# Optimization experiments

Hardware: AMD Instinct MI355X
Metric: run time of the kernel (lower is better)

The kernel has to match this reference:

```python
import jax, jax.numpy as jnp
import numpy as np

N = 20000   # nodes
E = 200000  # edges
D = 32      # inp_dim == out_dim == emb_dim
R = 100     # num_rel
EPS = 1e-5  # BatchNorm1d default eps


def setup_inputs() -> dict:
    key = jax.random.key(0)
    ks = jax.random.split(key, 5)
    h = jax.random.normal(ks[0], (N, D), dtype=jnp.float32)
    # xavier_uniform-ish scale for [R, D, D] relation weights
    weight = jax.random.normal(ks[1], (R, D, D), dtype=jnp.float32) * (1.0 / np.sqrt(D))
    gamma = jnp.ones((D,), dtype=jnp.float32)
    beta = jnp.zeros((D,), dtype=jnp.float32)
    src = jax.random.randint(ks[2], (E,), 0, N, dtype=jnp.int32)
    dst = jax.random.randint(ks[3], (E,), 0, N, dtype=jnp.int32)
    etype = jax.random.randint(ks[4], (E,), 0, R, dtype=jnp.int32)
    return {"h": h, "weight": weight, "gamma": gamma, "beta": beta,
            "src": src, "dst": dst, "etype": etype}


def reference(h, weight, gamma, beta, src, dst, etype):
    # per-edge relation-weight gather: [E, D, D]
    w_e = weight[etype]
    # per-edge bmm (src feature row-vector @ relation matrix) + relu: [E, D]
    msg = jax.nn.relu(jnp.einsum('ed,edo->eo', h[src], w_e))
    # BatchNorm1d in training mode: batch stats over the edge dimension
    mu = jnp.mean(msg, axis=0)
    var = jnp.mean(jnp.square(msg - mu), axis=0)  # biased variance
    msg = (msg - mu) * jax.lax.rsqrt(var + EPS) * gamma + beta
    # segment-mean reduce of messages into destination nodes: [N, D]
    ssum = jax.ops.segment_sum(msg, dst, num_segments=N)
    cnt = jax.ops.segment_sum(jnp.ones((E,), msg.dtype), dst, num_segments=N)
    return ssum / jnp.maximum(cnt, 1.0)[:, None]
```

## Files before the change

### kernel.cpp

```cpp
#include <hip/hip_runtime.h>

#define D 32
#define EPS 1e-5f
#define TPB 256
#define NB 256
#define NSLOT 64


__global__ void hist3_kernel(const int* __restrict__ etype, const int* __restrict__ dst,
                             int E, int R, int chunk,
                             int* __restrict__ blockHistT,
                             int* __restrict__ cnt)
{
    __shared__ int lh[1024];
    for (int i = threadIdx.x; i < R; i += TPB) lh[i] = 0;
    __syncthreads();
    const int lo = blockIdx.x * chunk, hi = min(E, lo + chunk);
    for (int e = lo + threadIdx.x; e < hi; e += TPB) {
        atomicAdd(&lh[etype[e]], 1);
        atomicAdd(&cnt[dst[e]], 1);
    }
    __syncthreads();
    for (int r = threadIdx.x; r < R; r += TPB)
        blockHistT[r * NB + blockIdx.x] = lh[r];
}

__global__ __launch_bounds__(TPB)
void scanA_kernel(int* __restrict__ blockHistT, int* __restrict__ relTot)
{
    const int r = blockIdx.x;
    const int t = threadIdx.x;
    __shared__ int s[TPB];
    const int v = blockHistT[r * NB + t];
    s[t] = v;
    __syncthreads();
    for (int off = 1; off < TPB; off <<= 1) {
        const int u = (t >= off) ? s[t - off] : 0;
        __syncthreads();
        s[t] += u;
        __syncthreads();
    }
    blockHistT[r * NB + t] = s[t] - v;
    if (t == TPB - 1) relTot[r] = s[t];
}

__global__ __launch_bounds__(1024)
void scanB_kernel(const int* __restrict__ relTot, int R, int E, int N,
                  int* __restrict__ rel_start,
                  int* __restrict__ task_rel, int* __restrict__ task_start,
                  int* __restrict__ n_tasks,
                  const int* __restrict__ cnt,
                  int* __restrict__ dst_base, int* __restrict__ cursor_dst)
{
    const int t = threadIdx.x;
    __shared__ int sa[1024];
    __shared__ int sc[1024];
    __shared__ int sb[1024];

    const int tot = (t < R) ? relTot[t] : 0;
    const int nb  = (tot + TPB - 1) / TPB;
    sa[t] = tot; sc[t] = nb;
    __syncthreads();
    for (int off = 1; off < 1024; off <<= 1) {
        const int va = (t >= off) ? sa[t - off] : 0;
        const int vc = (t >= off) ? sc[t - off] : 0;
        __syncthreads();
        sa[t] += va; sc[t] += vc;
        __syncthreads();
    }
    if (t < R) {
        const int st = sa[t] - tot;
        const int tb = sc[t] - nb;
        rel_start[t] = st;
        for (int b = 0; b < nb; ++b) {
            task_rel[tb + b]   = t;
            task_start[tb + b] = st + b * TPB;
        }
    }
    if (t == R - 1) {
        rel_start[R] = sa[t];
        *n_tasks = sc[t];
    }

    const int chunk = (N + 1023) >> 10;
    const int lo = t * chunk, hi = min(N, lo + chunk);
    int part = 0;
    for (int i = lo; i < hi; ++i) part += cnt[i];
    sb[t] = part;
    __syncthreads();
    for (int off = 1; off < 1024; off <<= 1) {
        const int v = (t >= off) ? sb[t - off] : 0;
        __syncthreads();
        sb[t] += v;
        __syncthreads();
    }
    int base = sb[t] - part;
    for (int i = lo; i < hi; ++i) {
        dst_base[i]   = base;
        cursor_dst[i] = base;
        base += cnt[i];
    }
    if (t == 0) dst_base[N] = E;
}

__global__ void scatter3_kernel(const int* __restrict__ src, const int* __restrict__ dst,
                                const int* __restrict__ etype, int E, int R, int chunk,
                                const int* __restrict__ blockHistT,
                                const int* __restrict__ rel_start,
                                int* __restrict__ cursor_dst,
                                int* __restrict__ ssrc, int* __restrict__ perm)
{
    __shared__ int cur[1024];
    for (int r = threadIdx.x; r < R; r += TPB)
        cur[r] = rel_start[r] + blockHistT[r * NB + blockIdx.x];
    __syncthreads();
    const int lo = blockIdx.x * chunk, hi = min(E, lo + chunk);
    for (int e = lo + threadIdx.x; e < hi; e += TPB) {
        const int p = atomicAdd(&cur[etype[e]], 1);
        ssrc[p] = src[e];
        const int q = atomicAdd(&cursor_dst[dst[e]], 1);
        perm[q] = p;
    }
}

__global__ __launch_bounds__(TPB)
void rgcn_main3(const float* __restrict__ h, const float* __restrict__ W,
                const int* __restrict__ rel_start,
                const int* __restrict__ task_rel, const int* __restrict__ task_start,
                const int* __restrict__ n_tasks_p,
                const int* __restrict__ ssrc,
                float* __restrict__ msg,
                float* __restrict__ stat_part)
{
    __shared__ float s_tile[TPB * 33];
    __shared__ int   s_src[TPB];
    __shared__ float s_aux[2 * TPB];

    const int task = blockIdx.x;
    if (task >= *n_tasks_p) return;
    const int r      = task_rel[task];
    const int start  = task_start[task];
    const int relEnd = rel_start[r + 1];
    const int nE     = min(TPB, relEnd - start);
    const int tid    = threadIdx.x;

    if (tid < nE) s_src[tid] = ssrc[start + tid];
    __syncthreads();

    for (int i = tid; i < nE * 8; i += TPB) {
        const int row = i >> 3, seg = i & 7;
        const float4 v = *(const float4*)(h + (size_t)s_src[row] * D + seg * 4);
        float* p = &s_tile[row * 33 + seg * 4];
        p[0] = v.x; p[1] = v.y; p[2] = v.z; p[3] = v.w;
    }
    __syncthreads();

    const float* Wr = W + (size_t)__builtin_amdgcn_readfirstlane(r) * (D * D);

    float acc[D];
#pragma unroll
    for (int o = 0; o < D; ++o) acc[o] = 0.f;

    if (tid < nE) {
#pragma unroll 4
        for (int d = 0; d < D; ++d) {
            const float hd = s_tile[tid * 33 + d];
#pragma unroll
            for (int o = 0; o < D; ++o)
                acc[o] = fmaf(hd, Wr[d * D + o], acc[o]);
        }
#pragma unroll
        for (int o = 0; o < D; ++o) acc[o] = fmaxf(acc[o], 0.f);
    }
    __syncthreads();

    if (tid < nE) {
#pragma unroll
        for (int o = 0; o < D; ++o) s_tile[tid * 33 + o] = acc[o];
    }
    __syncthreads();

    float* mbase = msg + (size_t)start * D;
    float ps = 0.f, pq = 0.f;
    for (int i = tid; i < nE * D; i += TPB) {
        const int row = i >> 5, o = i & 31;
        const float v = s_tile[row * 33 + o];
        mbase[i] = v;
        ps += v; pq += v * v;
    }
    s_aux[tid]       = ps;
    s_aux[TPB + tid] = pq;
    __syncthreads();
    if (tid < D) {
        float ss = 0.f, sq = 0.f;
#pragma unroll
        for (int c = 0; c < TPB / D; ++c) {
            ss += s_aux[c * D + tid];
            sq += s_aux[TPB + c * D + tid];
        }
        float* sp = stat_part + (size_t)(blockIdx.x & (NSLOT - 1)) * (2 * D);
        atomicAdd(&sp[tid],     ss);
        atomicAdd(&sp[D + tid], sq);
    }
}

__global__ __launch_bounds__(TPB)
void reduce3_kernel(const float* __restrict__ msg, const int* __restrict__ perm,
                    const int* __restrict__ dst_base,
                    const float* __restrict__ stat_part,
                    const float* __restrict__ gamma, const float* __restrict__ beta,
                    float invE, int N, float* __restrict__ out)
{
    __shared__ float s_sc[D], s_sh[D];
    const int tid = threadIdx.x;
    if (tid < D) {
        float ss = 0.f, qq = 0.f;
#pragma unroll 4
        for (int s = 0; s < NSLOT; ++s) {
            ss += stat_part[(size_t)s * (2 * D) + tid];
            qq += stat_part[(size_t)s * (2 * D) + D + tid];
        }
        const float mu  = ss * invE;
        const float var = fmaxf(qq * invE - mu * mu, 0.f);
        const float is  = rsqrtf(var + EPS);
        const float sc  = gamma[tid] * is;
        s_sc[tid] = sc;
        s_sh[tid] = fmaf(-mu, sc, beta[tid]);
    }
    __syncthreads();
    const int o    = tid & (D - 1);
    const int node = blockIdx.x * (TPB / D) + (tid >> 5);
    if (node >= N) return;
    const int b0 = dst_base[node], b1 = dst_base[node + 1];
    float v = 0.f;
    for (int q = b0; q < b1; ++q) {
        const int pe = perm[q];
        v += msg[(size_t)pe * D + o];
    }
    const float c = (float)(b1 - b0);
    out[(size_t)node * D + o] = fmaf(v, s_sc[o], s_sh[o] * c) / fmaxf(c, 1.0f);
}


__global__ void hist2_kernel(const int* __restrict__ etype, int E, int R, int chunk,
                             int* __restrict__ blockHistT)
{
    __shared__ int lh[1024];
    for (int i = threadIdx.x; i < R; i += TPB) lh[i] = 0;
    __syncthreads();
    const int lo = blockIdx.x * chunk, hi = min(E, lo + chunk);
    for (int e = lo + threadIdx.x; e < hi; e += TPB)
        atomicAdd(&lh[etype[e]], 1);
    __syncthreads();
    for (int r = threadIdx.x; r < R; r += TPB)
        blockHistT[r * NB + blockIdx.x] = lh[r];
}

__global__ void scan2_kernel(int* __restrict__ blockHistT, int R,
                             int* __restrict__ rel_start,
                             int* __restrict__ task_rel, int* __restrict__ task_start,
                             int* __restrict__ n_tasks)
{
    __shared__ int tot[1024];
    __shared__ int s_start[1025];
    __shared__ int s_tbase[1024];
    const int r = threadIdx.x;
    if (r < R) {
        int acc = 0;
        int* p = blockHistT + r * NB;
        for (int b = 0; b < NB; ++b) { int v = p[b]; p[b] = acc; acc += v; }
        tot[r] = acc;
    }
    __syncthreads();
    if (threadIdx.x == 0) {
        int acc = 0, tb = 0;
        for (int rr = 0; rr < R; ++rr) {
            s_start[rr] = acc; s_tbase[rr] = tb;
            acc += tot[rr];
            tb  += (tot[rr] + TPB - 1) / TPB;
        }
        s_start[R] = acc;
        rel_start[R] = acc;
        *n_tasks = tb;
    }
    __syncthreads();
    if (r < R) {
        const int st = s_start[r];
        rel_start[r] = st;
        const int nb = (tot[r] + TPB - 1) / TPB;
        const int tb = s_tbase[r];
        for (int b = 0; b < nb; ++b) {
            task_rel[tb + b]   = r;
            task_start[tb + b] = st + b * TPB;
        }
    }
}

__global__ void scatter2_kernel(const int* __restrict__ src, const int* __restrict__ dst,
                                const int* __restrict__ etype, int E, int R, int chunk,
                                const int* __restrict__ blockHistT,
                                const int* __restrict__ rel_start,
                                int* __restrict__ ssrc, int* __restrict__ sdst)
{
    __shared__ int cur[1024];
    for (int r = threadIdx.x; r < R; r += TPB)
        cur[r] = rel_start[r] + blockHistT[r * NB + blockIdx.x];
    __syncthreads();
    const int lo = blockIdx.x * chunk, hi = min(E, lo + chunk);
    for (int e = lo + threadIdx.x; e < hi; e += TPB) {
        const int p = atomicAdd(&cur[etype[e]], 1);
        ssrc[p] = src[e];
        sdst[p] = dst[e];
    }
}

__global__ __launch_bounds__(TPB)
void rgcn_main(const float* __restrict__ h, const float* __restrict__ W,
               const int* __restrict__ rel_start,
               const int* __restrict__ task_rel, const int* __restrict__ task_start,
               const int* __restrict__ n_tasks_p,
               const int* __restrict__ ssrc, const int* __restrict__ sdst,
               float* __restrict__ out,
               float* __restrict__ stat_sum, float* __restrict__ stat_sq,
               float* __restrict__ cnt)
{
    __shared__ float s_tile[TPB * 33];
    __shared__ int   s_src[TPB];
    __shared__ int   s_dst[TPB];
    __shared__ float s_aux[2 * TPB];

    const int task = blockIdx.x;
    if (task >= *n_tasks_p) return;
    const int r      = task_rel[task];
    const int start  = task_start[task];
    const int relEnd = rel_start[r + 1];
    const int nE     = min(TPB, relEnd - start);
    const int tid    = threadIdx.x;

    if (tid < nE) {
        s_src[tid] = ssrc[start + tid];
        s_dst[tid] = sdst[start + tid];
    }
    __syncthreads();

    for (int i = tid; i < nE * 8; i += TPB) {
        const int row = i >> 3, seg = i & 7;
        const float4 v = *(const float4*)(h + (size_t)s_src[row] * D + seg * 4);
        float* p = &s_tile[row * 33 + seg * 4];
        p[0] = v.x; p[1] = v.y; p[2] = v.z; p[3] = v.w;
    }
    __syncthreads();

    const float* Wr = W + (size_t)__builtin_amdgcn_readfirstlane(r) * (D * D);

    float acc[D];
#pragma unroll
    for (int o = 0; o < D; ++o) acc[o] = 0.f;

    if (tid < nE) {
#pragma unroll 4
        for (int d = 0; d < D; ++d) {
            const float hd = s_tile[tid * 33 + d];
#pragma unroll
            for (int o = 0; o < D; ++o)
                acc[o] = fmaf(hd, Wr[d * D + o], acc[o]);
        }
#pragma unroll
        for (int o = 0; o < D; ++o) acc[o] = fmaxf(acc[o], 0.f);
        atomicAdd(&cnt[s_dst[tid]], 1.0f);
    }
    __syncthreads();

    if (tid < nE) {
#pragma unroll
        for (int o = 0; o < D; ++o) s_tile[tid * 33 + o] = acc[o];
    }
    __syncthreads();

    float ps = 0.f, pq = 0.f;
    for (int i = tid; i < nE * D; i += TPB) {
        const int row = i >> 5, o = i & 31;
        const float v = s_tile[row * 33 + o];
        atomicAdd(&out[(size_t)s_dst[row] * D + o], v);
        ps += v; pq += v * v;
    }
    s_aux[tid]       = ps;
    s_aux[TPB + tid] = pq;
    __syncthreads();
    if (tid < D) {
        float ss = 0.f, sq = 0.f;
#pragma unroll
        for (int c = 0; c < TPB / D; ++c) {
            ss += s_aux[c * D + tid];
            sq += s_aux[TPB + c * D + tid];
        }
        atomicAdd(&stat_sum[tid], ss);
        atomicAdd(&stat_sq[tid], sq);
    }
}

__global__ void finalize_kernel(float* __restrict__ out, const float* __restrict__ cnt,
                                const float* __restrict__ stat_sum,
                                const float* __restrict__ stat_sq,
                                const float* __restrict__ gamma,
                                const float* __restrict__ beta,
                                float invE, int total)
{
    const int i = blockIdx.x * TPB + threadIdx.x;
    if (i >= total) return;
    const int o    = i & 31;
    const int node = i >> 5;
    const float mu  = stat_sum[o] * invE;
    const float var = fmaxf(stat_sq[o] * invE - mu * mu, 0.f);
    const float is  = rsqrtf(var + EPS);
    const float sc  = gamma[o] * is;
    const float sh  = fmaf(-mu, sc, beta[o]);
    const float c   = cnt[node];
    out[i] = fmaf(out[i], sc, sh * c) / fmaxf(c, 1.0f);
}

extern "C" void kernel_launch(void* const* d_in, const int* in_sizes, int n_in,
                              void* d_out, int out_size, void* d_ws, size_t ws_size,
                              hipStream_t stream)
{
    const float* h     = (const float*)d_in[0];
    const float* W     = (const float*)d_in[1];
    const float* gamma = (const float*)d_in[2];
    const float* beta  = (const float*)d_in[3];
    const int*   src   = (const int*)d_in[4];
    const int*   dst   = (const int*)d_in[5];
    const int*   etype = (const int*)d_in[6];
    float* out = (float*)d_out;

    const int E = in_sizes[4];
    const int N = in_sizes[0] / D;
    const int R = in_sizes[1] / (D * D);
    const int T = R + (E + TPB - 1) / TPB;
    const int chunk = (E + NB - 1) / NB;

    const size_t o_statp      = 0;
    const size_t o_cnt        = o_statp + (size_t)NSLOT * 2 * D;
    const size_t zwords       = o_cnt + (size_t)N;
    const size_t o_relTot     = zwords;
    const size_t o_rel_start  = o_relTot + R;
    const size_t o_n_tasks    = o_rel_start + R + 1;
    const size_t o_task_rel   = o_n_tasks + 1;
    const size_t o_task_start = o_task_rel + T;
    const size_t o_blockHistT = o_task_start + T;
    const size_t o_dst_base   = o_blockHistT + (size_t)R * NB;
    const size_t o_cursor_dst = o_dst_base + N + 1;
    const size_t o_ssrc       = o_cursor_dst + N;
    const size_t o_perm       = o_ssrc + (size_t)E;
    const size_t o_msg        = (o_perm + (size_t)E + 3) & ~(size_t)3;
    const size_t total_words  = o_msg + (size_t)E * D;

    if (R >= 1 && R <= 1024 && NB == TPB && ws_size >= total_words * 4) {
        float* stat_part  = (float*)d_ws + o_statp;
        int*   cnt        = (int*)d_ws + o_cnt;
        int*   relTot     = (int*)d_ws + o_relTot;
        int*   rel_start  = (int*)d_ws + o_rel_start;
        int*   n_tasks    = (int*)d_ws + o_n_tasks;
        int*   task_rel   = (int*)d_ws + o_task_rel;
        int*   task_start = (int*)d_ws + o_task_start;
        int*   blockHistT = (int*)d_ws + o_blockHistT;
        int*   dst_base   = (int*)d_ws + o_dst_base;
        int*   cursor_dst = (int*)d_ws + o_cursor_dst;
        int*   ssrc       = (int*)d_ws + o_ssrc;
        int*   perm       = (int*)d_ws + o_perm;
        float* msg        = (float*)d_ws + o_msg;

        hipMemsetAsync(d_ws, 0, zwords * 4, stream);

        hist3_kernel<<<NB, TPB, 0, stream>>>(etype, dst, E, R, chunk,
                                             blockHistT, cnt);
        scanA_kernel<<<R, TPB, 0, stream>>>(blockHistT, relTot);
        scanB_kernel<<<1, 1024, 0, stream>>>(relTot, R, E, N,
                                             rel_start, task_rel, task_start,
                                             n_tasks, cnt, dst_base, cursor_dst);
        scatter3_kernel<<<NB, TPB, 0, stream>>>(src, dst, etype, E, R, chunk,
                                                blockHistT, rel_start,
                                                cursor_dst, ssrc, perm);
        rgcn_main3<<<T, TPB, 0, stream>>>(h, W, rel_start, task_rel, task_start,
                                          n_tasks, ssrc, msg, stat_part);
        reduce3_kernel<<<(N + TPB / D - 1) / (TPB / D), TPB, 0, stream>>>(
            msg, perm, dst_base, stat_part, gamma, beta,
            1.0f / (float)E, N, out);
        return;
    }

    float* stat_sum  = (float*)d_ws;
    float* stat_sq   = stat_sum + D;
    float* cntf      = stat_sq + D;
    int*   rel_start = (int*)(cntf + N);
    int*   n_tasks   = rel_start + R + 1;
    int*   task_rel  = n_tasks + 1;
    int*   task_start= task_rel + T;
    int*   blockHistT= task_start + T;
    int*   ssrc      = blockHistT + R * NB;
    int*   sdst      = ssrc + E;

    hipMemsetAsync(d_ws, 0, sizeof(float) * (size_t)(2 * D + N), stream);
    hipMemsetAsync(d_out, 0, sizeof(float) * (size_t)out_size, stream);

    hist2_kernel<<<NB, TPB, 0, stream>>>(etype, E, R, chunk, blockHistT);
    scan2_kernel<<<1, TPB, 0, stream>>>(blockHistT, R, rel_start,
                                        task_rel, task_start, n_tasks);
    scatter2_kernel<<<NB, TPB, 0, stream>>>(src, dst, etype, E, R, chunk,
                                            blockHistT, rel_start, ssrc, sdst);
    rgcn_main<<<T, TPB, 0, stream>>>(h, W, rel_start, task_rel, task_start,
                                     n_tasks, ssrc, sdst, out,
                                     stat_sum, stat_sq, cntf);
    finalize_kernel<<<(N * D + TPB - 1) / TPB, TPB, 0, stream>>>(
        out, cntf, stat_sum, stat_sq, gamma, beta, 1.0f / (float)E, N * D);
}
```

Baseline: 183.1 us.

## Scatter messages into dst-sorted order and fuse relation scans into one kernel

The main kernel now writes each message row directly to its destination-sorted slot, using a position recorded during the scatter pass. The reduce kernel can then read contiguous rows without the perm indirection. The two-kernel relation scan is also merged into the single-block scan kernel, where 4 threads per relation do serial partial sums, which removes one launch. Writes from the main kernel become scattered 128-byte rows instead of contiguous ones, and the fast path now requires R <= 256.

```diff
diff --git a/kernel.cpp b/kernel.cpp
--- a/kernel.cpp
+++ b/kernel.cpp
@@ -25,27 +25,8 @@
         blockHistT[r * NB + blockIdx.x] = lh[r];
 }
 
-__global__ __launch_bounds__(TPB)
-void scanA_kernel(int* __restrict__ blockHistT, int* __restrict__ relTot)
-{
-    const int r = blockIdx.x;
-    const int t = threadIdx.x;
-    __shared__ int s[TPB];
-    const int v = blockHistT[r * NB + t];
-    s[t] = v;
-    __syncthreads();
-    for (int off = 1; off < TPB; off <<= 1) {
-        const int u = (t >= off) ? s[t - off] : 0;
-        __syncthreads();
-        s[t] += u;
-        __syncthreads();
-    }
-    blockHistT[r * NB + t] = s[t] - v;
-    if (t == TPB - 1) relTot[r] = s[t];
-}
-
 __global__ __launch_bounds__(1024)
-void scanB_kernel(const int* __restrict__ relTot, int R, int E, int N,
+void scanF_kernel(int* __restrict__ blockHistT, int R, int E, int N,
                   int* __restrict__ rel_start,
                   int* __restrict__ task_rel, int* __restrict__ task_start,
                   int* __restrict__ n_tasks,
@@ -53,11 +34,33 @@
                   int* __restrict__ dst_base, int* __restrict__ cursor_dst)
 {
     const int t = threadIdx.x;
+    __shared__ int qsum[1024];
     __shared__ int sa[1024];
     __shared__ int sc[1024];
     __shared__ int sb[1024];
 
-    const int tot = (t < R) ? relTot[t] : 0;
+    const int r = t >> 2, qt = t & 3;
+    int qs = 0;
+    if (r < R) {
+        const int base = r * NB + qt * (NB / 4);
+        for (int b = 0; b < NB / 4; ++b) qs += blockHistT[base + b];
+    }
+    qsum[t] = qs;
+    __syncthreads();
+
+    if (r < R) {
+        int acc = 0;
+        for (int k = 0; k < qt; ++k) acc += qsum[(r << 2) + k];
+        const int base = r * NB + qt * (NB / 4);
+        for (int b = 0; b < NB / 4; ++b) {
+            const int v = blockHistT[base + b];
+            blockHistT[base + b] = acc;
+            acc += v;
+        }
+    }
+
+    const int tot = (t < R) ? (qsum[t << 2] + qsum[(t << 2) + 1] +
+                               qsum[(t << 2) + 2] + qsum[(t << 2) + 3]) : 0;
     const int nb  = (tot + TPB - 1) / TPB;
     sa[t] = tot; sc[t] = nb;
     __syncthreads();
@@ -94,21 +97,21 @@
         sb[t] += v;
         __syncthreads();
     }
-    int base = sb[t] - part;
+    int base2 = sb[t] - part;
     for (int i = lo; i < hi; ++i) {
-        dst_base[i]   = base;
-        cursor_dst[i] = base;
-        base += cnt[i];
+        dst_base[i]   = base2;
+        cursor_dst[i] = base2;
+        base2 += cnt[i];
     }
     if (t == 0) dst_base[N] = E;
 }
 
-__global__ void scatter3_kernel(const int* __restrict__ src, const int* __restrict__ dst,
+__global__ void scatter4_kernel(const int* __restrict__ src, const int* __restrict__ dst,
                                 const int* __restrict__ etype, int E, int R, int chunk,
                                 const int* __restrict__ blockHistT,
                                 const int* __restrict__ rel_start,
                                 int* __restrict__ cursor_dst,
-                                int* __restrict__ ssrc, int* __restrict__ perm)
+                                int* __restrict__ ssrc, int* __restrict__ tpos)
 {
     __shared__ int cur[1024];
     for (int r = threadIdx.x; r < R; r += TPB)
@@ -118,22 +121,22 @@
     for (int e = lo + threadIdx.x; e < hi; e += TPB) {
         const int p = atomicAdd(&cur[etype[e]], 1);
         ssrc[p] = src[e];
-        const int q = atomicAdd(&cursor_dst[dst[e]], 1);
-        perm[q] = p;
+        tpos[p] = atomicAdd(&cursor_dst[dst[e]], 1);
     }
 }
 
 __global__ __launch_bounds__(TPB)
-void rgcn_main3(const float* __restrict__ h, const float* __restrict__ W,
-                const int* __restrict__ rel_start,
-                const int* __restrict__ task_rel, const int* __restrict__ task_start,
-                const int* __restrict__ n_tasks_p,
-                const int* __restrict__ ssrc,
-                float* __restrict__ msg,
-                float* __restrict__ stat_part)
+void main4_kernel(const float* __restrict__ h, const float* __restrict__ W,
+                  const int* __restrict__ rel_start,
+                  const int* __restrict__ task_rel, const int* __restrict__ task_start,
+                  const int* __restrict__ n_tasks_p,
+                  const int* __restrict__ ssrc, const int* __restrict__ tpos,
+                  float* __restrict__ msg,
+                  float* __restrict__ stat_part)
 {
     __shared__ float s_tile[TPB * 33];
     __shared__ int   s_src[TPB];
+    __shared__ int   s_tpos[TPB];
     __shared__ float s_aux[2 * TPB];
 
     const int task = blockIdx.x;
@@ -144,7 +147,10 @@
     const int nE     = min(TPB, relEnd - start);
     const int tid    = threadIdx.x;
 
-    if (tid < nE) s_src[tid] = ssrc[start + tid];
+    if (tid < nE) {
+        s_src[tid]  = ssrc[start + tid];
+        s_tpos[tid] = tpos[start + tid];
+    }
     __syncthreads();
 
     for (int i = tid; i < nE * 8; i += TPB) {
@@ -180,12 +186,11 @@
     }
     __syncthreads();
 
-    float* mbase = msg + (size_t)start * D;
     float ps = 0.f, pq = 0.f;
     for (int i = tid; i < nE * D; i += TPB) {
         const int row = i >> 5, o = i & 31;
         const float v = s_tile[row * 33 + o];
-        mbase[i] = v;
+        msg[(size_t)s_tpos[row] * D + o] = v;
         ps += v; pq += v * v;
     }
     s_aux[tid]       = ps;
@@ -205,7 +210,7 @@
 }
 
 __global__ __launch_bounds__(TPB)
-void reduce3_kernel(const float* __restrict__ msg, const int* __restrict__ perm,
+void reduceS_kernel(const float* __restrict__ msg,
                     const int* __restrict__ dst_base,
                     const float* __restrict__ stat_part,
                     const float* __restrict__ gamma, const float* __restrict__ beta,
@@ -233,10 +238,8 @@
     if (node >= N) return;
     const int b0 = dst_base[node], b1 = dst_base[node + 1];
     float v = 0.f;
-    for (int q = b0; q < b1; ++q) {
-        const int pe = perm[q];
-        v += msg[(size_t)pe * D + o];
-    }
+    for (int q = b0; q < b1; ++q)
+        v += msg[(size_t)q * D + o];
     const float c = (float)(b1 - b0);
     out[(size_t)node * D + o] = fmaf(v, s_sc[o], s_sh[o] * c) / fmaxf(c, 1.0f);
 }
@@ -441,8 +444,7 @@
     const size_t o_statp      = 0;
     const size_t o_cnt        = o_statp + (size_t)NSLOT * 2 * D;
     const size_t zwords       = o_cnt + (size_t)N;
-    const size_t o_relTot     = zwords;
-    const size_t o_rel_start  = o_relTot + R;
+    const size_t o_rel_start  = zwords;
     const size_t o_n_tasks    = o_rel_start + R + 1;
     const size_t o_task_rel   = o_n_tasks + 1;
     const size_t o_task_start = o_task_rel + T;
@@ -450,14 +452,13 @@
     const size_t o_dst_base   = o_blockHistT + (size_t)R * NB;
     const size_t o_cursor_dst = o_dst_base + N + 1;
     const size_t o_ssrc       = o_cursor_dst + N;
-    const size_t o_perm       = o_ssrc + (size_t)E;
-    const size_t o_msg        = (o_perm + (size_t)E + 3) & ~(size_t)3;
+    const size_t o_tpos       = o_ssrc + (size_t)E;
+    const size_t o_msg        = (o_tpos + (size_t)E + 3) & ~(size_t)3;
     const size_t total_words  = o_msg + (size_t)E * D;
 
-    if (R >= 1 && R <= 1024 && NB == TPB && ws_size >= total_words * 4) {
+    if (R >= 1 && R <= 256 && NB == TPB && ws_size >= total_words * 4) {
         float* stat_part  = (float*)d_ws + o_statp;
         int*   cnt        = (int*)d_ws + o_cnt;
-        int*   relTot     = (int*)d_ws + o_relTot;
         int*   rel_start  = (int*)d_ws + o_rel_start;
         int*   n_tasks    = (int*)d_ws + o_n_tasks;
         int*   task_rel   = (int*)d_ws + o_task_rel;
@@ -466,25 +467,23 @@
         int*   dst_base   = (int*)d_ws + o_dst_base;
         int*   cursor_dst = (int*)d_ws + o_cursor_dst;
         int*   ssrc       = (int*)d_ws + o_ssrc;
-        int*   perm       = (int*)d_ws + o_perm;
+        int*   tpos       = (int*)d_ws + o_tpos;
         float* msg        = (float*)d_ws + o_msg;
 
         hipMemsetAsync(d_ws, 0, zwords * 4, stream);
 
         hist3_kernel<<<NB, TPB, 0, stream>>>(etype, dst, E, R, chunk,
                                              blockHistT, cnt);
-        scanA_kernel<<<R, TPB, 0, stream>>>(blockHistT, relTot);
-        scanB_kernel<<<1, 1024, 0, stream>>>(relTot, R, E, N,
+        scanF_kernel<<<1, 1024, 0, stream>>>(blockHistT, R, E, N,
                                              rel_start, task_rel, task_start,
                                              n_tasks, cnt, dst_base, cursor_dst);
-        scatter3_kernel<<<NB, TPB, 0, stream>>>(src, dst, etype, E, R, chunk,
+        scatter4_kernel<<<NB, TPB, 0, stream>>>(src, dst, etype, E, R, chunk,
                                                 blockHistT, rel_start,
-                                                cursor_dst, ssrc, perm);
-        rgcn_main3<<<T, TPB, 0, stream>>>(h, W, rel_start, task_rel, task_start,
-                                          n_tasks, ssrc, msg, stat_part);
-        reduce3_kernel<<<(N + TPB / D - 1) / (TPB / D), TPB, 0, stream>>>(
-            msg, perm, dst_base, stat_part, gamma, beta,
-            1.0f / (float)E, N, out);
+                                                cursor_dst, ssrc, tpos);
+        main4_kernel<<<T, TPB, 0, stream>>>(h, W, rel_start, task_rel, task_start,
+                                            n_tasks, ssrc, tpos, msg, stat_part);
+        reduceS_kernel<<<(N + TPB / D - 1) / (TPB / D), TPB, 0, stream>>>(
+            msg, dst_base, stat_part, gamma, beta, 1.0f / (float)E, N, out);
         return;
     }
 
```

Result: no change. 182.3 us (-0.5%).
